# Kernel tuning notes

Measured on AMD Instinct MI355X. Metric: run time of the kernel, lower is better.

Reference implementation:

```python
import jax, jax.numpy as jnp
import numpy as np

RADIUS = 2.0  # ball-query radius (float forward arg in the original; fixed here)


def _conv1x1(x, W, b):
    # 1x1 Conv2D over NHWC == per-point linear layer
    return jnp.einsum('bmsc,cd->bmsd', x, W) + b


def _ball_query(xyz, new_xyz, radius, nsample):
    """For each cluster center, take the first (by index) nsample points within
    radius, padding with the first found neighbor (TF ball-query semantics).
    xyz: (B,N,3), new_xyz: (B,M,3) -> idx (B,M,nsample) int32."""
    N = xyz.shape[1]
    d2 = jnp.sum((new_xyz[:, :, None, :] - xyz[:, None, :, :]) ** 2, axis=-1)  # (B,M,N)
    valid = d2 < radius * radius
    key = jnp.where(valid, jnp.arange(N, dtype=jnp.int32)[None, None, :], N)
    order = jnp.argsort(key, axis=-1)[..., :nsample]          # (B,M,nsample)
    skey = jnp.take_along_axis(key, order, axis=-1)
    idx = jnp.where(skey < N, order, order[..., :1])          # pad with first neighbor
    return idx


def setup_inputs() -> dict:
    key = jax.random.key(0)
    ks = jax.random.split(key, 8)
    B, N = 8, 8192
    xyz = jax.random.normal(ks[0], (B, N, 3), dtype=jnp.float32)

    def w(k, cin, cout):
        return (jax.random.normal(k, (cin, cout), dtype=jnp.float32) / np.sqrt(cin)).astype(jnp.float32)

    z = lambda c: jnp.zeros((c,), jnp.float32)
    inp = {
        'xyz': xyz,
        'W1': w(ks[1], 3, 64),    'b1': z(64),
        'W2': w(ks[2], 64, 128),  'b2': z(128),
        'W3': w(ks[3], 128, 256), 'b3': z(256),
        'W4': w(ks[4], 256, 128), 'b4': z(128),
        'W5': w(ks[5], 128, 64),  'b5': z(64),
        'Wa': w(ks[6], 64, 1),    'ba': z(1),
        'Wo': w(ks[7], 64, 2),    'bo': z(2),
        'num_clusters': 512,
        'num_samples': 64,
    }
    return inp


def reference(xyz, W1, b1, W2, b2, W3, b3, W4, b4, W5, b5, Wa, ba, Wo, bo,
              num_clusters, num_samples):
    # sample cluster centers (deterministic stand-in for random subsampling)
    new_xyz = xyz[:, :num_clusters]                                    # (B,M,3)
    idx = _ball_query(xyz, new_xyz, RADIUS, num_samples)               # (B,M,S)
    grouped = jax.vmap(lambda pts, i: pts[i])(xyz, idx)                # (B,M,S,3)
    g = (grouped - new_xyz[:, :, None, :]) / RADIUS                    # normalize_radius

    # shared per-point MLP (1x1 convs, relu)
    h = jax.nn.relu(_conv1x1(g, W1, b1))
    h = jax.nn.relu(_conv1x1(h, W2, b2))
    h = jax.nn.relu(_conv1x1(h, W3, b3))
    # MaxPoolAxis: max over samples, keepdims
    h = jnp.max(h, axis=2, keepdims=True)                              # (B,M,1,256)
    # mlp2 convs (linear, no activation in source)
    h = _conv1x1(h, W4, b4)
    h = _conv1x1(h, W5, b5)                                            # (B,M,1,64)

    attention = jax.nn.softplus(_conv1x1(h, Wa, ba))[:, :, 0, 0]       # (B,M)
    o = _conv1x1(h, Wo, bo)[:, :, 0, :]                                # (B,M,2)
    o = o / jnp.sqrt(jnp.maximum(jnp.sum(o * o, axis=-1, keepdims=True), 1e-8))
    orientation = jnp.arctan2(o[..., 1], o[..., 0])                    # (B,M)
    return new_xyz, idx, attention, orientation
```

## Files before the change

kernel.cpp:

```cpp
#include <hip/hip_runtime.h>
#include <math.h>

#define BB 8
#define NN 8192
#define MM 512
#define SS 64
#define NCLUST (BB*MM)

#define OUT_IDX   (BB*MM*3)
#define OUT_ATT   (OUT_IDX + BB*MM*SS)
#define OUT_ORI   (OUT_ATT + BB*MM)

#define WS_W3 8192

typedef short v8s __attribute__((ext_vector_type(8)));
typedef float v4f __attribute__((ext_vector_type(4)));

static __device__ __forceinline__ unsigned short f2bf(float x) {
    unsigned int u = __float_as_uint(x);
    u += 0x7FFFu + ((u >> 16) & 1u);
    return (unsigned short)(u >> 16);
}

__global__ void pack_weights(const float* __restrict__ W2,
                             const float* __restrict__ W3,
                             unsigned short* __restrict__ ws)
{
    const int gid = blockIdx.x * 256 + threadIdx.x;
    const float* W; unsigned short* dst; int N, kt, nt, lane;
    if (gid < 1024) {
        W = W2; N = 128;
        const int tile = gid >> 6; lane = gid & 63;
        kt = tile >> 3; nt = tile & 7;
        dst = ws + (size_t)(tile * 64 + lane) * 8;
    } else {
        const int g = gid - 1024;
        W = W3; N = 256;
        const int tile = g >> 6; lane = g & 63;
        kt = tile >> 4; nt = tile & 15;
        dst = ws + WS_W3 + (size_t)(tile * 64 + lane) * 8;
    }
    const int k0 = kt * 32 + (lane >> 4) * 8;
    const int n  = nt * 16 + (lane & 15);
    union { unsigned short u[8]; v8s v; } f;
    #pragma unroll
    for (int j = 0; j < 8; ++j) f.u[j] = f2bf(W[(k0 + j) * N + n]);
    *(v8s*)dst = f.v;
}

__global__ __launch_bounds__(256, 4) void feat3d_fused(
    const float* __restrict__ xyz,
    const float* __restrict__ W1, const float* __restrict__ b1,
    const float* __restrict__ b2, const float* __restrict__ b3,
    const unsigned short* __restrict__ Wp,
    const float* __restrict__ W4, const float* __restrict__ b4,
    const float* __restrict__ W5, const float* __restrict__ b5,
    const float* __restrict__ Wa, const float* __restrict__ ba,
    const float* __restrict__ Wo, const float* __restrict__ bo,
    float* __restrict__ out)
{
    __shared__ __align__(16) unsigned char lds[27200];
    unsigned short* a2p = (unsigned short*)lds;
    unsigned short* a3p = (unsigned short*)(lds + 8192);
    float* smallf       = (float*)(lds + 24576);
    int* ls_idx         = (int*)(lds + 26624);
    unsigned long long* ls_mask = (unsigned long long*)(lds + 26880);

    float* ls_g  = smallf;
    float* ls_w1 = smallf + 256;

    float* vbuf = (float*)lds;
    float* h4p  = (float*)(lds + 1024);
    float* h4f  = (float*)(lds + 2048);
    float* h5p  = (float*)(lds + 2560);

    const int t   = threadIdx.x;
    const int wv  = t >> 6;
    const int l   = t & 63;
    const int q   = l >> 4;
    const int r16 = l & 15;
    const int blk = blockIdx.x;
    const int b   = blk >> 9;
    const int m   = blk & 511;
    const float* xb = xyz + (size_t)b * (NN * 3);

    const v8s* W2f = (const v8s*)Wp;
    v8s bfr[2][2];
    #pragma unroll
    for (int kt = 0; kt < 2; ++kt)
        #pragma unroll
        for (int ni = 0; ni < 2; ++ni)
            bfr[kt][ni] = W2f[(kt*8 + 2*wv + ni)*64 + l];

    const float cx = xb[m*3+0], cy = xb[m*3+1], cz = xb[m*3+2];

    if (t < 3) out[(b*MM + m)*3 + t] = xb[m*3 + t];

    if (t < 64) {
        ls_w1[t*4+0] = W1[t];
        ls_w1[t*4+1] = W1[64 + t];
        ls_w1[t*4+2] = W1[128 + t];
        ls_w1[t*4+3] = b1[t];
    }

    int cnt = 0;
    {
        int base = 0, pb = 0;
        while (base < NN && cnt < SS) {
            const int j = base + t;
            const float dx = xb[j*3+0] - cx;
            const float dy = xb[j*3+1] - cy;
            const float dz = xb[j*3+2] - cz;
            const float d2 = __fadd_rn(__fadd_rn(__fmul_rn(dx,dx), __fmul_rn(dy,dy)),
                                       __fmul_rn(dz,dz));
            const bool valid = d2 < 4.0f;
            const unsigned long long mask = __ballot(valid);
            if (l == 0) ls_mask[pb*4 + wv] = mask;
            __syncthreads();
            const unsigned long long m0 = ls_mask[pb*4+0], m1 = ls_mask[pb*4+1],
                                     m2 = ls_mask[pb*4+2], m3 = ls_mask[pb*4+3];
            int below = __popcll(mask & ((1ull << l) - 1ull));
            if (wv > 0) below += (int)__popcll(m0);
            if (wv > 1) below += (int)__popcll(m1);
            if (wv > 2) below += (int)__popcll(m2);
            const int pos = cnt + below;
            if (valid && pos < SS) {
                ls_idx[pos]   = j;
                ls_g[pos*4+0] = dx * 0.5f;
                ls_g[pos*4+1] = dy * 0.5f;
                ls_g[pos*4+2] = dz * 0.5f;
            }
            cnt += (int)(__popcll(m0) + __popcll(m1) + __popcll(m2) + __popcll(m3));
            if (cnt > SS) cnt = SS;
            base += 256;
            pb ^= 1;
        }
    }
    __syncthreads();
    if (t < SS && t >= cnt) {
        ls_idx[t]   = ls_idx[0];
        ls_g[t*4+0] = ls_g[0];
        ls_g[t*4+1] = ls_g[1];
        ls_g[t*4+2] = ls_g[2];
    }
    __syncthreads();
    if (t < 64) out[OUT_IDX + (b*MM + m)*SS + t] = (float)ls_idx[t];

    {
        const int s = wv*16 + r16;
        const float4 g4 = *(const float4*)&ls_g[s*4];
        #pragma unroll
        for (int kt = 0; kt < 2; ++kt) {
            union { unsigned short u[8]; v8s v; } fr;
            #pragma unroll
            for (int j = 0; j < 8; ++j) {
                const int c = kt*32 + q*8 + j;
                const float4 w = *(const float4*)&ls_w1[c*4];
                const float h = fmaf(g4.x, w.x, fmaf(g4.y, w.y, fmaf(g4.z, w.z, w.w)));
                fr.u[j] = f2bf(fmaxf(h, 0.f));
            }
            *(v8s*)&a2p[((kt*4 + wv)*64 + l)*8] = fr.v;
        }
    }
    __syncthreads();

    {
        const v4f z = {0.f, 0.f, 0.f, 0.f};
        v4f acc[4][2];
        #pragma unroll
        for (int mt = 0; mt < 4; ++mt) { acc[mt][0] = z; acc[mt][1] = z; }

        #pragma unroll
        for (int kt = 0; kt < 2; ++kt)
            #pragma unroll
            for (int mt = 0; mt < 4; ++mt) {
                const v8s a = *(const v8s*)&a2p[((kt*4 + mt)*64 + l)*8];
                #pragma unroll
                for (int ni = 0; ni < 2; ++ni)
                    acc[mt][ni] = __builtin_amdgcn_mfma_f32_16x16x32_bf16(
                        a, bfr[kt][ni], acc[mt][ni], 0, 0, 0);
            }

        #pragma unroll
        for (int ni = 0; ni < 2; ++ni) {
            const int c2  = (2*wv + ni)*16 + r16;
            const float bias = b2[c2];
            const int kt3 = c2 >> 5;
            const int lhi = ((c2 >> 3) & 3) << 4;
            const int j3  = c2 & 7;
            #pragma unroll
            for (int mt = 0; mt < 4; ++mt)
                #pragma unroll
                for (int rg = 0; rg < 4; ++rg) {
                    const float h = fmaxf(acc[mt][ni][rg] + bias, 0.f);
                    const int s15 = q*4 + rg;
                    a3p[((kt3*4 + mt)*64 + (lhi | s15))*8 + j3] = f2bf(h);
                }
        }
    }
    __syncthreads();

    {
        const v8s* W3f = (const v8s*)(Wp + WS_W3);

        #pragma unroll
        for (int np = 0; np < 2; ++np) {
            const int nt0 = 4*wv + 2*np;
            const v4f z = {0.f, 0.f, 0.f, 0.f};
            v4f acc[4][2];
            #pragma unroll
            for (int mt = 0; mt < 4; ++mt) { acc[mt][0] = z; acc[mt][1] = z; }

            v8s bb0 = W3f[(0*16 + nt0    )*64 + l];
            v8s bb1 = W3f[(0*16 + nt0 + 1)*64 + l];
            #pragma unroll
            for (int kt = 0; kt < 4; ++kt) {
                v8s a[4];
                #pragma unroll
                for (int mt = 0; mt < 4; ++mt)
                    a[mt] = *(const v8s*)&a3p[((kt*4 + mt)*64 + l)*8];
                v8s nb0, nb1;
                if (kt < 3) {
                    nb0 = W3f[((kt+1)*16 + nt0    )*64 + l];
                    nb1 = W3f[((kt+1)*16 + nt0 + 1)*64 + l];
                }
                #pragma unroll
                for (int mt = 0; mt < 4; ++mt) {
                    acc[mt][0] = __builtin_amdgcn_mfma_f32_16x16x32_bf16(
                        a[mt], bb0, acc[mt][0], 0, 0, 0);
                    acc[mt][1] = __builtin_amdgcn_mfma_f32_16x16x32_bf16(
                        a[mt], bb1, acc[mt][1], 0, 0, 0);
                }
                if (kt < 3) { bb0 = nb0; bb1 = nb1; }
            }

            #pragma unroll
            for (int ni = 0; ni < 2; ++ni) {
                float mx = acc[0][ni][0];
                #pragma unroll
                for (int mt = 0; mt < 4; ++mt)
                    #pragma unroll
                    for (int rg = 0; rg < 4; ++rg)
                        mx = fmaxf(mx, acc[mt][ni][rg]);
                mx = fmaxf(mx, __shfl_xor(mx, 16));
                mx = fmaxf(mx, __shfl_xor(mx, 32));
                if (q == 0) {
                    const int c = (nt0 + ni)*16 + r16;
                    vbuf[c] = fmaxf(mx + b3[c], 0.f);
                }
            }
        }
    }
    __syncthreads();

    {
        const int c4 = t & 127;
        const int kh = t >> 7;
        const float* W4c = W4 + c4;
        float acc = 0.f;
        for (int k = kh*128; k < kh*128 + 128; k += 4) {
            const float4 vv = *(const float4*)&vbuf[k];
            acc = fmaf(vv.x, W4c[(k+0)*128],
                  fmaf(vv.y, W4c[(k+1)*128],
                  fmaf(vv.z, W4c[(k+2)*128],
                  fmaf(vv.w, W4c[(k+3)*128], acc))));
        }
        h4p[t] = acc;
    }
    __syncthreads();
    if (t < 128) h4f[t] = h4p[t] + h4p[128 + t] + b4[t];
    __syncthreads();

    {
        const int c5 = t & 63;
        const int kq = t >> 6;
        const float* W5c = W5 + c5;
        float acc = 0.f;
        for (int k = kq*32; k < kq*32 + 32; k += 4) {
            const float4 hh = *(const float4*)&h4f[k];
            acc = fmaf(hh.x, W5c[(k+0)*64],
                  fmaf(hh.y, W5c[(k+1)*64],
                  fmaf(hh.z, W5c[(k+2)*64],
                  fmaf(hh.w, W5c[(k+3)*64], acc))));
        }
        h5p[t] = acc;
    }
    __syncthreads();

    if (t < 64) {
        const float h5v = h5p[t] + h5p[64 + t] + h5p[128 + t] + h5p[192 + t] + b5[t];
        float va = h5v * Wa[t];
        float v0 = h5v * Wo[2*t + 0];
        float v1 = h5v * Wo[2*t + 1];
        #pragma unroll
        for (int off = 32; off > 0; off >>= 1) {
            va += __shfl_down(va, off);
            v0 += __shfl_down(v0, off);
            v1 += __shfl_down(v1, off);
        }
        if (t == 0) {
            const float a = va + ba[0];
            out[OUT_ATT + blk] = fmaxf(a, 0.f) + log1pf(expf(-fabsf(a)));
            out[OUT_ORI + blk] = atan2f(v1 + bo[1], v0 + bo[0]);
        }
    }
}

extern "C" void kernel_launch(void* const* d_in, const int* in_sizes, int n_in,
                              void* d_out, int out_size, void* d_ws, size_t ws_size,
                              hipStream_t stream) {
    const float* xyz = (const float*)d_in[0];
    const float* W1  = (const float*)d_in[1];
    const float* b1  = (const float*)d_in[2];
    const float* W2  = (const float*)d_in[3];
    const float* b2  = (const float*)d_in[4];
    const float* W3  = (const float*)d_in[5];
    const float* b3  = (const float*)d_in[6];
    const float* W4  = (const float*)d_in[7];
    const float* b4  = (const float*)d_in[8];
    const float* W5  = (const float*)d_in[9];
    const float* b5  = (const float*)d_in[10];
    const float* Wa  = (const float*)d_in[11];
    const float* ba  = (const float*)d_in[12];
    const float* Wo  = (const float*)d_in[13];
    const float* bo  = (const float*)d_in[14];

    unsigned short* ws = (unsigned short*)d_ws;

    pack_weights<<<dim3(20), dim3(256), 0, stream>>>(W2, W3, ws);
    feat3d_fused<<<dim3(NCLUST), dim3(256), 0, stream>>>(
        xyz, W1, b1, b2, b3, ws, W4, b4, W5, b5, Wa, ba, Wo, bo, (float*)d_out);
}
```

Baseline: 134.3 us.

## Process four clusters per block to amortize W4/W5 weight reads

Each block now handles four cluster centers in sequence through ball query and the MFMA MLP, storing the four pooled 256-wide features in LDS. The W4 and W5 GEMVs then run once, batched over all four clusters, so each weight element is loaded once per four clusters instead of once per cluster. The grid shrinks by 4x. The cost is that each block runs the ball-query and MLP phases serially, and there are fewer blocks to balance load across CUs.

```diff
diff --git a/kernel.cpp b/kernel.cpp
--- a/kernel.cpp
+++ b/kernel.cpp
@@ -6,6 +6,7 @@
 #define MM 512
 #define SS 64
 #define NCLUST (BB*MM)
+#define CPB 4
 
 #define OUT_IDX   (BB*MM*3)
 #define OUT_ATT   (OUT_IDX + BB*MM*SS)
@@ -59,20 +60,20 @@
     const float* __restrict__ Wo, const float* __restrict__ bo,
     float* __restrict__ out)
 {
-    __shared__ __align__(16) unsigned char lds[27200];
+    __shared__ __align__(16) unsigned char lds[31040];
     unsigned short* a2p = (unsigned short*)lds;
     unsigned short* a3p = (unsigned short*)(lds + 8192);
     float* smallf       = (float*)(lds + 24576);
     int* ls_idx         = (int*)(lds + 26624);
     unsigned long long* ls_mask = (unsigned long long*)(lds + 26880);
+    float* vbuf         = (float*)(lds + 26944);
 
     float* ls_g  = smallf;
     float* ls_w1 = smallf + 256;
 
-    float* vbuf = (float*)lds;
-    float* h4p  = (float*)(lds + 1024);
-    float* h4f  = (float*)(lds + 2048);
-    float* h5p  = (float*)(lds + 2560);
+    float* h5part = (float*)lds;
+    float* h4part = (float*)(lds + 8192);
+    float* h4f    = (float*)(lds + 24576);
 
     const int t   = threadIdx.x;
     const int wv  = t >> 6;
@@ -80,8 +81,8 @@
     const int q   = l >> 4;
     const int r16 = l & 15;
     const int blk = blockIdx.x;
-    const int b   = blk >> 9;
-    const int m   = blk & 511;
+    const int b   = blk >> 7;
+    const int m0  = (blk & 127) * CPB;
     const float* xb = xyz + (size_t)b * (NN * 3);
 
     const v8s* W2f = (const v8s*)Wp;
@@ -91,10 +92,6 @@
         #pragma unroll
         for (int ni = 0; ni < 2; ++ni)
             bfr[kt][ni] = W2f[(kt*8 + 2*wv + ni)*64 + l];
-
-    const float cx = xb[m*3+0], cy = xb[m*3+1], cz = xb[m*3+2];
-
-    if (t < 3) out[(b*MM + m)*3 + t] = xb[m*3 + t];
 
     if (t < 64) {
         ls_w1[t*4+0] = W1[t];
@@ -103,150 +100,159 @@
         ls_w1[t*4+3] = b1[t];
     }
 
-    int cnt = 0;
-    {
-        int base = 0, pb = 0;
-        while (base < NN && cnt < SS) {
-            const int j = base + t;
-            const float dx = xb[j*3+0] - cx;
-            const float dy = xb[j*3+1] - cy;
-            const float dz = xb[j*3+2] - cz;
-            const float d2 = __fadd_rn(__fadd_rn(__fmul_rn(dx,dx), __fmul_rn(dy,dy)),
-                                       __fmul_rn(dz,dz));
-            const bool valid = d2 < 4.0f;
-            const unsigned long long mask = __ballot(valid);
-            if (l == 0) ls_mask[pb*4 + wv] = mask;
-            __syncthreads();
-            const unsigned long long m0 = ls_mask[pb*4+0], m1 = ls_mask[pb*4+1],
-                                     m2 = ls_mask[pb*4+2], m3 = ls_mask[pb*4+3];
-            int below = __popcll(mask & ((1ull << l) - 1ull));
-            if (wv > 0) below += (int)__popcll(m0);
-            if (wv > 1) below += (int)__popcll(m1);
-            if (wv > 2) below += (int)__popcll(m2);
-            const int pos = cnt + below;
-            if (valid && pos < SS) {
-                ls_idx[pos]   = j;
-                ls_g[pos*4+0] = dx * 0.5f;
-                ls_g[pos*4+1] = dy * 0.5f;
-                ls_g[pos*4+2] = dz * 0.5f;
-            }
-            cnt += (int)(__popcll(m0) + __popcll(m1) + __popcll(m2) + __popcll(m3));
-            if (cnt > SS) cnt = SS;
-            base += 256;
-            pb ^= 1;
-        }
-    }
-    __syncthreads();
-    if (t < SS && t >= cnt) {
-        ls_idx[t]   = ls_idx[0];
-        ls_g[t*4+0] = ls_g[0];
-        ls_g[t*4+1] = ls_g[1];
-        ls_g[t*4+2] = ls_g[2];
-    }
-    __syncthreads();
-    if (t < 64) out[OUT_IDX + (b*MM + m)*SS + t] = (float)ls_idx[t];
-
-    {
-        const int s = wv*16 + r16;
-        const float4 g4 = *(const float4*)&ls_g[s*4];
-        #pragma unroll
-        for (int kt = 0; kt < 2; ++kt) {
-            union { unsigned short u[8]; v8s v; } fr;
-            #pragma unroll
-            for (int j = 0; j < 8; ++j) {
-                const int c = kt*32 + q*8 + j;
-                const float4 w = *(const float4*)&ls_w1[c*4];
-                const float h = fmaf(g4.x, w.x, fmaf(g4.y, w.y, fmaf(g4.z, w.z, w.w)));
-                fr.u[j] = f2bf(fmaxf(h, 0.f));
-            }
-            *(v8s*)&a2p[((kt*4 + wv)*64 + l)*8] = fr.v;
-        }
-    }
-    __syncthreads();
-
-    {
-        const v4f z = {0.f, 0.f, 0.f, 0.f};
-        v4f acc[4][2];
-        #pragma unroll
-        for (int mt = 0; mt < 4; ++mt) { acc[mt][0] = z; acc[mt][1] = z; }
-
-        #pragma unroll
-        for (int kt = 0; kt < 2; ++kt)
-            #pragma unroll
-            for (int mt = 0; mt < 4; ++mt) {
-                const v8s a = *(const v8s*)&a2p[((kt*4 + mt)*64 + l)*8];
-                #pragma unroll
-                for (int ni = 0; ni < 2; ++ni)
-                    acc[mt][ni] = __builtin_amdgcn_mfma_f32_16x16x32_bf16(
-                        a, bfr[kt][ni], acc[mt][ni], 0, 0, 0);
-            }
-
-        #pragma unroll
-        for (int ni = 0; ni < 2; ++ni) {
-            const int c2  = (2*wv + ni)*16 + r16;
-            const float bias = b2[c2];
-            const int kt3 = c2 >> 5;
-            const int lhi = ((c2 >> 3) & 3) << 4;
-            const int j3  = c2 & 7;
-            #pragma unroll
-            for (int mt = 0; mt < 4; ++mt)
-                #pragma unroll
-                for (int rg = 0; rg < 4; ++rg) {
-                    const float h = fmaxf(acc[mt][ni][rg] + bias, 0.f);
-                    const int s15 = q*4 + rg;
-                    a3p[((kt3*4 + mt)*64 + (lhi | s15))*8 + j3] = f2bf(h);
-                }
-        }
-    }
-    __syncthreads();
-
-    {
-        const v8s* W3f = (const v8s*)(Wp + WS_W3);
-
-        #pragma unroll
-        for (int np = 0; np < 2; ++np) {
-            const int nt0 = 4*wv + 2*np;
+    #pragma unroll 1
+    for (int ci = 0; ci < CPB; ++ci) {
+        const int m  = m0 + ci;
+        const int cg = b*MM + m;
+
+        const float cx = xb[m*3+0], cy = xb[m*3+1], cz = xb[m*3+2];
+        if (t < 3) out[cg*3 + t] = xb[m*3 + t];
+
+        int cnt = 0;
+        {
+            int base = 0, pb = 0;
+            while (base < NN && cnt < SS) {
+                const int j = base + t;
+                const float dx = xb[j*3+0] - cx;
+                const float dy = xb[j*3+1] - cy;
+                const float dz = xb[j*3+2] - cz;
+                const float d2 = __fadd_rn(__fadd_rn(__fmul_rn(dx,dx), __fmul_rn(dy,dy)),
+                                           __fmul_rn(dz,dz));
+                const bool valid = d2 < 4.0f;
+                const unsigned long long mask = __ballot(valid);
+                if (l == 0) ls_mask[pb*4 + wv] = mask;
+                __syncthreads();
+                const unsigned long long mk0 = ls_mask[pb*4+0], mk1 = ls_mask[pb*4+1],
+                                         mk2 = ls_mask[pb*4+2], mk3 = ls_mask[pb*4+3];
+                int below = __popcll(mask & ((1ull << l) - 1ull));
+                if (wv > 0) below += (int)__popcll(mk0);
+                if (wv > 1) below += (int)__popcll(mk1);
+                if (wv > 2) below += (int)__popcll(mk2);
+                const int pos = cnt + below;
+                if (valid && pos < SS) {
+                    ls_idx[pos]   = j;
+                    ls_g[pos*4+0] = dx * 0.5f;
+                    ls_g[pos*4+1] = dy * 0.5f;
+                    ls_g[pos*4+2] = dz * 0.5f;
+                }
+                cnt += (int)(__popcll(mk0) + __popcll(mk1) + __popcll(mk2) + __popcll(mk3));
+                if (cnt > SS) cnt = SS;
+                base += 256;
+                pb ^= 1;
+            }
+        }
+        __syncthreads();
+        if (t < SS && t >= cnt) {
+            ls_idx[t]   = ls_idx[0];
+            ls_g[t*4+0] = ls_g[0];
+            ls_g[t*4+1] = ls_g[1];
+            ls_g[t*4+2] = ls_g[2];
+        }
+        __syncthreads();
+        if (t < 64) out[OUT_IDX + cg*SS + t] = (float)ls_idx[t];
+
+        {
+            const int s = wv*16 + r16;
+            const float4 g4 = *(const float4*)&ls_g[s*4];
+            #pragma unroll
+            for (int kt = 0; kt < 2; ++kt) {
+                union { unsigned short u[8]; v8s v; } fr;
+                #pragma unroll
+                for (int j = 0; j < 8; ++j) {
+                    const int c = kt*32 + q*8 + j;
+                    const float4 w = *(const float4*)&ls_w1[c*4];
+                    const float h = fmaf(g4.x, w.x, fmaf(g4.y, w.y, fmaf(g4.z, w.z, w.w)));
+                    fr.u[j] = f2bf(fmaxf(h, 0.f));
+                }
+                *(v8s*)&a2p[((kt*4 + wv)*64 + l)*8] = fr.v;
+            }
+        }
+        __syncthreads();
+
+        {
             const v4f z = {0.f, 0.f, 0.f, 0.f};
             v4f acc[4][2];
             #pragma unroll
             for (int mt = 0; mt < 4; ++mt) { acc[mt][0] = z; acc[mt][1] = z; }
 
-            v8s bb0 = W3f[(0*16 + nt0    )*64 + l];
-            v8s bb1 = W3f[(0*16 + nt0 + 1)*64 + l];
-            #pragma unroll
-            for (int kt = 0; kt < 4; ++kt) {
-                v8s a[4];
+            #pragma unroll
+            for (int kt = 0; kt < 2; ++kt)
+                #pragma unroll
+                for (int mt = 0; mt < 4; ++mt) {
+                    const v8s a = *(const v8s*)&a2p[((kt*4 + mt)*64 + l)*8];
+                    #pragma unroll
+                    for (int ni = 0; ni < 2; ++ni)
+                        acc[mt][ni] = __builtin_amdgcn_mfma_f32_16x16x32_bf16(
+                            a, bfr[kt][ni], acc[mt][ni], 0, 0, 0);
+                }
+
+            #pragma unroll
+            for (int ni = 0; ni < 2; ++ni) {
+                const int c2  = (2*wv + ni)*16 + r16;
+                const float bias = b2[c2];
+                const int kt3 = c2 >> 5;
+                const int lhi = ((c2 >> 3) & 3) << 4;
+                const int j3  = c2 & 7;
                 #pragma unroll
                 for (int mt = 0; mt < 4; ++mt)
-                    a[mt] = *(const v8s*)&a3p[((kt*4 + mt)*64 + l)*8];
-                v8s nb0, nb1;
-                if (kt < 3) {
-                    nb0 = W3f[((kt+1)*16 + nt0    )*64 + l];
-                    nb1 = W3f[((kt+1)*16 + nt0 + 1)*64 + l];
-                }
-                #pragma unroll
-                for (int mt = 0; mt < 4; ++mt) {
-                    acc[mt][0] = __builtin_amdgcn_mfma_f32_16x16x32_bf16(
-                        a[mt], bb0, acc[mt][0], 0, 0, 0);
-                    acc[mt][1] = __builtin_amdgcn_mfma_f32_16x16x32_bf16(
-                        a[mt], bb1, acc[mt][1], 0, 0, 0);
-                }
-                if (kt < 3) { bb0 = nb0; bb1 = nb1; }
-            }
-
-            #pragma unroll
-            for (int ni = 0; ni < 2; ++ni) {
-                float mx = acc[0][ni][0];
-                #pragma unroll
-                for (int mt = 0; mt < 4; ++mt)
-                    #pragma unroll
-                    for (int rg = 0; rg < 4; ++rg)
-                        mx = fmaxf(mx, acc[mt][ni][rg]);
-                mx = fmaxf(mx, __shfl_xor(mx, 16));
-                mx = fmaxf(mx, __shfl_xor(mx, 32));
-                if (q == 0) {
-                    const int c = (nt0 + ni)*16 + r16;
-                    vbuf[c] = fmaxf(mx + b3[c], 0.f);
+                    #pragma unroll
+                    for (int rg = 0; rg < 4; ++rg) {
+                        const float h = fmaxf(acc[mt][ni][rg] + bias, 0.f);
+                        const int s15 = q*4 + rg;
+                        a3p[((kt3*4 + mt)*64 + (lhi | s15))*8 + j3] = f2bf(h);
+                    }
+            }
+        }
+        __syncthreads();
+
+        {
+            const v8s* W3f = (const v8s*)(Wp + WS_W3);
+
+            #pragma unroll
+            for (int np = 0; np < 2; ++np) {
+                const int nt0 = 4*wv + 2*np;
+                const v4f z = {0.f, 0.f, 0.f, 0.f};
+                v4f acc[4][2];
+                #pragma unroll
+                for (int mt = 0; mt < 4; ++mt) { acc[mt][0] = z; acc[mt][1] = z; }
+
+                v8s bb0 = W3f[(0*16 + nt0    )*64 + l];
+                v8s bb1 = W3f[(0*16 + nt0 + 1)*64 + l];
+                #pragma unroll
+                for (int kt = 0; kt < 4; ++kt) {
+                    v8s a[4];
+                    #pragma unroll
+                    for (int mt = 0; mt < 4; ++mt)
+                        a[mt] = *(const v8s*)&a3p[((kt*4 + mt)*64 + l)*8];
+                    v8s nb0, nb1;
+                    if (kt < 3) {
+                        nb0 = W3f[((kt+1)*16 + nt0    )*64 + l];
+                        nb1 = W3f[((kt+1)*16 + nt0 + 1)*64 + l];
+                    }
+                    #pragma unroll
+                    for (int mt = 0; mt < 4; ++mt) {
+                        acc[mt][0] = __builtin_amdgcn_mfma_f32_16x16x32_bf16(
+                            a[mt], bb0, acc[mt][0], 0, 0, 0);
+                        acc[mt][1] = __builtin_amdgcn_mfma_f32_16x16x32_bf16(
+                            a[mt], bb1, acc[mt][1], 0, 0, 0);
+                    }
+                    if (kt < 3) { bb0 = nb0; bb1 = nb1; }
+                }
+
+                #pragma unroll
+                for (int ni = 0; ni < 2; ++ni) {
+                    float mx = acc[0][ni][0];
+                    #pragma unroll
+                    for (int mt = 0; mt < 4; ++mt)
+                        #pragma unroll
+                        for (int rg = 0; rg < 4; ++rg)
+                            mx = fmaxf(mx, acc[mt][ni][rg]);
+                    mx = fmaxf(mx, __shfl_xor(mx, 16));
+                    mx = fmaxf(mx, __shfl_xor(mx, 32));
+                    if (q == 0) {
+                        const int c = (nt0 + ni)*16 + r16;
+                        vbuf[ci*256 + c] = fmaxf(mx + b3[c], 0.f);
+                    }
                 }
             }
         }
@@ -254,54 +260,78 @@
     __syncthreads();
 
     {
-        const int c4 = t & 127;
-        const int kh = t >> 7;
-        const float* W4c = W4 + c4;
-        float acc = 0.f;
-        for (int k = kh*128; k < kh*128 + 128; k += 4) {
-            const float4 vv = *(const float4*)&vbuf[k];
-            acc = fmaf(vv.x, W4c[(k+0)*128],
-                  fmaf(vv.y, W4c[(k+1)*128],
-                  fmaf(vv.z, W4c[(k+2)*128],
-                  fmaf(vv.w, W4c[(k+3)*128], acc))));
-        }
-        h4p[t] = acc;
+        const int cgp = t & 31;
+        const int kp  = t >> 5;
+        const float4* W4v = (const float4*)W4;
+        float4 acc[CPB];
+        #pragma unroll
+        for (int cl = 0; cl < CPB; ++cl) acc[cl] = make_float4(0.f, 0.f, 0.f, 0.f);
+        const int kbase = kp * 32;
+        #pragma unroll 4
+        for (int kk = 0; kk < 32; ++kk) {
+            const int k = kbase + kk;
+            const float4 w = W4v[k*32 + cgp];
+            #pragma unroll
+            for (int cl = 0; cl < CPB; ++cl) {
+                const float vv = vbuf[cl*256 + k];
+                acc[cl].x = fmaf(vv, w.x, acc[cl].x);
+                acc[cl].y = fmaf(vv, w.y, acc[cl].y);
+                acc[cl].z = fmaf(vv, w.z, acc[cl].z);
+                acc[cl].w = fmaf(vv, w.w, acc[cl].w);
+            }
+        }
+        #pragma unroll
+        for (int cl = 0; cl < CPB; ++cl)
+            *(float4*)&h4part[(kp*4 + cl)*128 + cgp*4] = acc[cl];
     }
     __syncthreads();
-    if (t < 128) h4f[t] = h4p[t] + h4p[128 + t] + b4[t];
+
+    #pragma unroll
+    for (int idx = t; idx < 512; idx += 256) {
+        const int cl = idx >> 7, c = idx & 127;
+        float s = b4[c];
+        #pragma unroll
+        for (int kp = 0; kp < 8; ++kp) s += h4part[(kp*4 + cl)*128 + c];
+        h4f[cl*128 + c] = s;
+    }
     __syncthreads();
 
     {
         const int c5 = t & 63;
         const int kq = t >> 6;
-        const float* W5c = W5 + c5;
-        float acc = 0.f;
-        for (int k = kq*32; k < kq*32 + 32; k += 4) {
-            const float4 hh = *(const float4*)&h4f[k];
-            acc = fmaf(hh.x, W5c[(k+0)*64],
-                  fmaf(hh.y, W5c[(k+1)*64],
-                  fmaf(hh.z, W5c[(k+2)*64],
-                  fmaf(hh.w, W5c[(k+3)*64], acc))));
-        }
-        h5p[t] = acc;
+        float acc5[CPB] = {0.f, 0.f, 0.f, 0.f};
+        #pragma unroll 4
+        for (int kk = 0; kk < 32; ++kk) {
+            const int k = kq*32 + kk;
+            const float w = W5[k*64 + c5];
+            #pragma unroll
+            for (int cl = 0; cl < CPB; ++cl)
+                acc5[cl] = fmaf(h4f[cl*128 + k], w, acc5[cl]);
+        }
+        #pragma unroll
+        for (int cl = 0; cl < CPB; ++cl)
+            h5part[(kq*4 + cl)*64 + c5] = acc5[cl];
     }
     __syncthreads();
 
-    if (t < 64) {
-        const float h5v = h5p[t] + h5p[64 + t] + h5p[128 + t] + h5p[192 + t] + b5[t];
-        float va = h5v * Wa[t];
-        float v0 = h5v * Wo[2*t + 0];
-        float v1 = h5v * Wo[2*t + 1];
+    {
+        float h5v = b5[l];
+        #pragma unroll
+        for (int kq = 0; kq < 4; ++kq) h5v += h5part[(kq*4 + wv)*64 + l];
+        float va = h5v * Wa[l];
+        float v0 = h5v * Wo[2*l + 0];
+        float v1 = h5v * Wo[2*l + 1];
         #pragma unroll
         for (int off = 32; off > 0; off >>= 1) {
             va += __shfl_down(va, off);
             v0 += __shfl_down(v0, off);
             v1 += __shfl_down(v1, off);
         }
-        if (t == 0) {
+        if (l == 0) {
+            const int cg = (b*MM + m0) + wv;
             const float a = va + ba[0];
-            out[OUT_ATT + blk] = fmaxf(a, 0.f) + log1pf(expf(-fabsf(a)));
-            out[OUT_ORI + blk] = atan2f(v1 + bo[1], v0 + bo[0]);
+            out[OUT_ATT + cg] = fmaxf(a, 0.f) + log1pf(expf(-fabsf(a)));
+            out[OUT_ORI + cg] = atan2f(v1 + bo[1], v0 + bo[0]);
         }
     }
 }
@@ -328,6 +358,6 @@
     unsigned short* ws = (unsigned short*)d_ws;
 
     pack_weights<<<dim3(20), dim3(256), 0, stream>>>(W2, W3, ws);
-    feat3d_fused<<<dim3(NCLUST), dim3(256), 0, stream>>>(
+    feat3d_fused<<<dim3(NCLUST/CPB), dim3(256), 0, stream>>>(
         xyz, W1, b1, b2, b3, ws, W4, b4, W5, b5, Wa, ba, Wo, bo, (float*)d_out);
 }
```

Measured after the change: 209.1 us. +55.7%, slower.
